# Kernel optimization log

Measured on AMD Instinct MI355X. Metric: run time of the kernel, lower is better.

The kernel has to match this reference:

```python
import jax, jax.numpy as jnp
import numpy as np

# Fixed problem geometry: B equal-sized graphs with contiguous node ids.
B, N, E, F_IN, H, C = 64, 1024, 655360, 128, 128, 10
K1 = int(np.ceil(0.8 * N))    # 820 nodes/graph kept by pool1
K2 = int(np.ceil(0.8 * K1))   # 656 nodes/graph kept by pool2


def setup_inputs() -> dict:
    key = jax.random.key(0)
    ks = jax.random.split(key, 12)
    x = jax.random.normal(ks[0], (B * N, F_IN), jnp.float32)
    # intra-graph random edges, E//B per graph
    e_per = E // B
    local = jax.random.randint(ks[1], (2, E), 0, N)
    off = jnp.repeat(jnp.arange(B, dtype=jnp.int32) * N, e_per)
    edge_index = (local + off[None, :]).astype(jnp.int32)
    batch = jnp.repeat(jnp.arange(B, dtype=jnp.int32), N)

    def lin(k, i, o):
        return jax.random.normal(k, (i, o), jnp.float32) / np.sqrt(i)

    return {
        "x": x, "edge_index": edge_index, "batch": batch,
        "Wl1": lin(ks[2], F_IN, H), "bl1": jnp.zeros((H,), jnp.float32), "Wr1": lin(ks[3], F_IN, H),
        "Wl2": lin(ks[4], H, H),    "bl2": jnp.zeros((H,), jnp.float32), "Wr2": lin(ks[5], H, H),
        "pw1": jax.random.normal(ks[6], (H,), jnp.float32) / np.sqrt(H),
        "pw2": jax.random.normal(ks[7], (H,), jnp.float32) / np.sqrt(H),
        "fW1": lin(ks[8], 2 * H, H), "fb1": jnp.zeros((H,), jnp.float32),
        "fW2": lin(ks[9], H, C),     "fb2": jnp.zeros((C,), jnp.float32),
    }


def _sage(x, src, dst, em, Wl, bl, Wr, n):
    # PyG SAGEConv (aggr='mean'): lin_l(mean_{j->i} x_j) + lin_r(x_i)
    msg = x[src] * em[:, None]                                   # [E, d]
    s = jax.ops.segment_sum(msg, dst, num_segments=n)            # [n, d]
    cnt = jax.ops.segment_sum(em, dst, num_segments=n)           # [n]
    mean = s / jnp.maximum(cnt, 1.0)[:, None]
    return mean @ Wl + bl + x @ Wr


def _topk_pool(x, src, dst, em, n_per, k, w):
    # PyG TopKPooling: score = tanh(x.w/||w||); keep top-k per graph; gate kept x by score.
    score = jnp.tanh(x @ w / jnp.linalg.norm(w))                 # [B*n_per]
    _, idx = jax.lax.top_k(score.reshape(B, n_per), k)           # [B, k]
    idx = jnp.sort(idx, axis=1)
    perm = (idx + (jnp.arange(B) * n_per)[:, None]).reshape(-1)  # global kept ids [B*k]
    nx = x[perm] * score[perm][:, None]
    # relabel edges; drop edges touching removed nodes via mask
    inv = jnp.full((B * n_per,), -1, jnp.int32).at[perm].set(jnp.arange(B * k, dtype=jnp.int32))
    ns, nd = inv[src], inv[dst]
    nm = em * (ns >= 0).astype(x.dtype) * (nd >= 0).astype(x.dtype)
    return nx, jnp.maximum(ns, 0), jnp.maximum(nd, 0), nm


def _readout(h, k):
    g = h.reshape(B, k, H)
    return jnp.concatenate([g.mean(axis=1), g.max(axis=1)], axis=1)  # [B, 2H]


def reference(x, edge_index, batch, Wl1, bl1, Wr1, Wl2, bl2, Wr2,
              pw1, pw2, fW1, fb1, fW2, fb2):
    src, dst = edge_index[0], edge_index[1]
    em = jnp.ones((E,), x.dtype)
    h = jax.nn.relu(_sage(x, src, dst, em, Wl1, bl1, Wr1, B * N))
    h, src, dst, em = _topk_pool(h, src, dst, em, N, K1, pw1)
    x1 = _readout(h, K1)
    h = jax.nn.relu(_sage(h, src, dst, em, Wl2, bl2, Wr2, B * K1))
    h, src, dst, em = _topk_pool(h, src, dst, em, K1, K2, pw2)
    x2 = _readout(h, K2)
    z = jax.nn.relu((x1 + x2) @ fW1 + fb1)
    # dropout is identity in eval mode
    return z @ fW2 + fb2
```

## Files before the change

kernel.cpp:

```cpp
#include <hip/hip_runtime.h>
#include <cstdint>
#include <cstddef>

namespace {

constexpr int kB    = 64;
constexpr int kN    = 1024;
constexpr int kE    = 655360;
constexpr int kEper = kE / kB;
constexpr int kH    = 128;
constexpr int kK1   = 820;
constexpr int kK2   = 656;
constexpr int kM1   = kB * kN;
constexpr int kM2   = kB * kK1;
constexpr int kM3   = kB * kK2;
constexpr int kRChunks = 16;

typedef __attribute__((ext_vector_type(8))) short bf16x8;
typedef __attribute__((ext_vector_type(4))) float f32x4;

__device__ inline ushort f2bf(float f) {
  uint u = __float_as_uint(f);
  return (ushort)((u + 0x7fffu + ((u >> 16) & 1u)) >> 16);
}
__device__ inline float bf2f(ushort s) { return __uint_as_float(((uint)s) << 16); }

__device__ inline void cvt4(const float* f, uint* hh, uint* ll) {
#pragma unroll
  for (int i = 0; i < 2; ++i) {
    uint h;
    asm("v_cvt_pk_bf16_f32 %0, %1, %2" : "=v"(h) : "v"(f[2 * i]), "v"(f[2 * i + 1]));
    const float r0 = __uint_as_float(h << 16);
    const float r1 = __uint_as_float(h & 0xFFFF0000u);
    const float d0 = f[2 * i] - r0;
    const float d1 = f[2 * i + 1] - r1;
    uint l;
    asm("v_cvt_pk_bf16_f32 %0, %1, %2" : "=v"(l) : "v"(d0), "v"(d1));
    hh[i] = h; ll[i] = l;
  }
}

__device__ inline void llds16(const ushort* g, ushort* l) {
  __builtin_amdgcn_global_load_lds(
      (const __attribute__((address_space(1))) void*)g,
      (__attribute__((address_space(3))) void*)l, 16, 0, 0);
}

__device__ inline int block_scan_1024(int v, int* wsum ) {
  const int lane = threadIdx.x & 63;
  const int w    = threadIdx.x >> 6;
#pragma unroll
  for (int off = 1; off < 64; off <<= 1) {
    const int n = __shfl_up(v, off);
    if (lane >= off) v += n;
  }
  if (lane == 63) wsum[w] = v;
  __syncthreads();
  if (w == 0) {
    int s = (lane < 16) ? wsum[lane] : 0;
#pragma unroll
    for (int off = 1; off < 16; off <<= 1) {
      const int n = __shfl_up(s, off);
      if (lane >= off) s += n;
    }
    if (lane < 16) wsum[lane] = s;
  }
  __syncthreads();
  if (w > 0) v += wsum[w - 1];
  return v;
}

__global__ __launch_bounds__(1024)
void build_prep(const int* __restrict__ src, const int* __restrict__ dst,
                int* __restrict__ coff, int* __restrict__ ccur,
                int* __restrict__ ent,
                const float* __restrict__ Wl1, const float* __restrict__ Wr1,
                const float* __restrict__ Wl2, const float* __restrict__ Wr2,
                const float* __restrict__ pw1, const float* __restrict__ pw2,
                ushort* __restrict__ W1h, ushort* __restrict__ W1l,
                ushort* __restrict__ W2h, ushort* __restrict__ W2l,
                float* __restrict__ pwn1, float* __restrict__ pwn2) {
  const int b   = blockIdx.x;
  const int tid = threadIdx.x;
  if (b >= 128) {
    if (tid >= 256) return;
    const float* pw = (tid < 128) ? pw1 : pw2;
    float* o        = (tid < 128) ? pwn1 : pwn2;
    const int j = tid & 127;
    float sum = 0.0f;
    for (int k = 0; k < 128; ++k) { const float v = pw[k]; sum += v * v; }
    o[j] = pw[j] / sqrtf(sum);
    return;
  }
  if (b >= 64) {
    const int ob  = (b - 64) * 4 + (tid >> 8);
    const bool l2 = ob >= 128;
    const int idx = (ob & 127) * 256 + (tid & 255);
    const int n = idx >> 8, k = idx & 255;
    const float* Wl = l2 ? Wl2 : Wl1;
    const float* Wr = l2 ? Wr2 : Wr1;
    const float w = (k < 128) ? Wl[k * kH + n] : Wr[(k - 128) * kH + n];
    const ushort h = f2bf(w);
    (l2 ? W2h : W1h)[n * 256 + k] = h;
    (l2 ? W2l : W1l)[n * 256 + k] = f2bf(w - bf2f(h));
    return;
  }
  __shared__ int cnt[1024];
  __shared__ int wsum[16];
  const int g = b;
  const int ebase = g * kEper;
  cnt[tid] = 0;
  __syncthreads();
  for (int e = tid; e < kEper; e += 1024)
    atomicAdd(&cnt[dst[ebase + e] & (kN - 1)], 1);
  __syncthreads();
  const int dg   = cnt[tid];
  const int incl = block_scan_1024(dg, wsum);
  const int start = ebase + incl - dg;
  coff[g * kN + tid] = start;
  ccur[g * kN + tid] = start + dg;
  __syncthreads();
  cnt[tid] = start;
  __syncthreads();
  for (int e = tid; e < kEper; e += 1024) {
    const int d   = dst[ebase + e] & (kN - 1);
    const int pos = atomicAdd(&cnt[d], 1);
    ent[pos] = src[ebase + e] & (kN - 1);
  }
}

__global__ __launch_bounds__(1024, 8)
void gather1_lds(const float* __restrict__ feat, const int* __restrict__ ent,
                 const int* __restrict__ off, const int* __restrict__ cursor,
                 float* __restrict__ aggout) {
  __shared__ float cache[1024 * 16];
  const int xcd   = blockIdx.x & 7;
  const int local = blockIdx.x >> 3;
  const int graph = xcd * 8 + (local >> 3);
  const int chunk = local & 7;
  const int tid   = threadIdx.x;
  const int gbase = graph << 10;

#pragma unroll
  for (int ps = 0; ps < 4; ++ps) {
    const int row = ps * 256 + (tid >> 2);
    const int q   = (tid & 3) * 4;
    const float4 v = *(const float4*)(feat + (size_t)(gbase + row) * kH + chunk * 16 + q);
    *(float4*)&cache[row * 16 + q] = v;
  }
  __syncthreads();

  const int grp = tid >> 2;
  const int q4  = (tid & 3) * 4;

  for (int it = 0; it < 4; ++it) {
    const int lnode = it * 256 + grp;
    const int node  = gbase + lnode;
    const int o0 = off[node];
    const int o1 = cursor[node];
    const int deg = o1 - o0;
    float4 acc = make_float4(0.f, 0.f, 0.f, 0.f);
    int pf[4];
#pragma unroll
    for (int i = 0; i < 4; ++i) pf[i] = (o0 + i < o1) ? ent[o0 + i] : 0;
    for (int eb = 0; eb < deg; eb += 4) {
      int nx[4];
#pragma unroll
      for (int i = 0; i < 4; ++i) {
        const int idx = o0 + eb + 4 + i;
        nx[i] = (idx < o1) ? ent[idx] : 0;
      }
#pragma unroll
      for (int i = 0; i < 4; ++i) {
        const float m = (eb + i < deg) ? 1.0f : 0.0f;
        const float4 v = *(const float4*)&cache[pf[i] * 16 + q4];
        acc.x = fmaf(v.x, m, acc.x);
        acc.y = fmaf(v.y, m, acc.y);
        acc.z = fmaf(v.z, m, acc.z);
        acc.w = fmaf(v.w, m, acc.w);
      }
#pragma unroll
      for (int i = 0; i < 4; ++i) pf[i] = nx[i];
    }
    const float r = 1.0f / fmaxf((float)deg, 1.0f);
    const f32x4 res = {acc.x * r, acc.y * r, acc.z * r, acc.w * r};
    __builtin_nontemporal_store(res, (f32x4*)(aggout + (size_t)node * kH + chunk * 16 + q4));
  }
}

__global__ __launch_bounds__(1024, 8)
void gather2_lds(const float* __restrict__ feat, const int* __restrict__ ent,
                 const int* __restrict__ off, const int* __restrict__ cursor,
                 const int* __restrict__ perm, const float* __restrict__ gsg,
                 float* __restrict__ aggout) {
  __shared__ float cache[1024 * 16];
  __shared__ float gs[1024];
  const int xcd   = blockIdx.x & 7;
  const int local = blockIdx.x >> 3;
  const int graph = xcd * 8 + (local >> 3);
  const int chunk = local & 7;
  const int tid   = threadIdx.x;
  const int gbase = graph << 10;

#pragma unroll
  for (int ps = 0; ps < 4; ++ps) {
    const int row = ps * 256 + (tid >> 2);
    const int q   = (tid & 3) * 4;
    const float4 v = *(const float4*)(feat + (size_t)(gbase + row) * kH + chunk * 16 + q);
    *(float4*)&cache[row * 16 + q] = v;
  }
  gs[tid] = gsg[gbase + tid];
  __syncthreads();

  const int grp = tid >> 2;
  const int q4  = (tid & 3) * 4;

  for (int it = 0; it < 4; ++it) {
    const int lnode = it * 256 + grp;
    int o0 = 0, o1 = 0;
    if (lnode < kK1) {
      const int orig = perm[graph * kK1 + lnode];
      o0 = off[orig];
      o1 = cursor[orig];
    }
    const int deg = o1 - o0;
    float4 acc = make_float4(0.f, 0.f, 0.f, 0.f);
    int cnt = 0;
    int pf[4];
#pragma unroll
    for (int i = 0; i < 4; ++i) pf[i] = (o0 + i < o1) ? ent[o0 + i] : 0;
    for (int eb = 0; eb < deg; eb += 4) {
      int nx[4];
#pragma unroll
      for (int i = 0; i < 4; ++i) {
        const int idx = o0 + eb + 4 + i;
        nx[i] = (idx < o1) ? ent[idx] : 0;
      }
#pragma unroll
      for (int i = 0; i < 4; ++i) {
        const float raw  = gs[pf[i]];
        const bool  kept = (raw > 0.5f) && (eb + i < deg);
        const float s    = kept ? raw - 2.0f : 0.0f;
        cnt += kept ? 1 : 0;
        const float4 v = *(const float4*)&cache[pf[i] * 16 + q4];
        acc.x = fmaf(v.x, s, acc.x);
        acc.y = fmaf(v.y, s, acc.y);
        acc.z = fmaf(v.z, s, acc.z);
        acc.w = fmaf(v.w, s, acc.w);
      }
#pragma unroll
      for (int i = 0; i < 4; ++i) pf[i] = nx[i];
    }
    const float r = 1.0f / fmaxf((float)cnt, 1.0f);
    const f32x4 res = {acc.x * r, acc.y * r, acc.z * r, acc.w * r};
    if (lnode < kK1)
      __builtin_nontemporal_store(res,
          (f32x4*)(aggout + (size_t)(graph * kK1 + lnode) * kH + chunk * 16 + q4));
  }
}

__global__ __launch_bounds__(256)
void sage_gemm_mfma(const float* __restrict__ meanb, const float* __restrict__ xsrc,
                    const int* __restrict__ perm, const float* __restrict__ gsc,
                    const ushort* __restrict__ WTh, const ushort* __restrict__ WTl,
                    const float* __restrict__ bias, const float* __restrict__ pwn,
                    float* __restrict__ outp, float* __restrict__ scr) {
  __shared__ __align__(16) ushort aH[64][32];
  __shared__ __align__(16) ushort aL[64][32];
  __shared__ __align__(16) ushort wHs[128][32];
  __shared__ __align__(16) ushort wLs[128][32];
  __shared__ float sdot[64][2];
  const int tid  = threadIdx.x;
  const int wid  = tid >> 6;
  const int lane = tid & 63;
  const int quad = lane >> 4;
  const int l16  = lane & 15;
  const int rowbase = blockIdx.x * 64;
  const int wr = (wid >> 1) * 32;
  const int wc = (wid & 1) * 64;

  const int n0a = wid * 32;
  const int n0b = wid * 32 + 16;
  const int wrowa = (n0a + (lane >> 2)) * 256 + (lane & 3) * 8;
  const int wrowb = (n0b + (lane >> 2)) * 256 + (lane & 3) * 8;

  f32x4 acc[2][4];
#pragma unroll
  for (int a = 0; a < 2; ++a)
#pragma unroll
    for (int b = 0; b < 4; ++b) acc[a][b] = (f32x4){0.f, 0.f, 0.f, 0.f};

  for (int s = 0; s < 8; ++s) {
    const bool ismean = s < 4;
    const float* sp = ismean ? meanb : xsrc;
    const int kbase = s * 32;
    const int kloc  = ismean ? kbase : kbase - 128;
#pragma unroll
    for (int i = 0; i < 2; ++i) {
      const int p   = tid + i * 256;
      const int row = p >> 3;
      const int k4  = (p & 7) * 4;
      const int grow = rowbase + row;
      int srow = grow; float scale = 1.0f;
      if (perm) { if (!ismean) { srow = perm[grow]; scale = gsc[grow]; } }
      const float4 v = *(const float4*)(sp + (size_t)srow * kH + kloc + k4);
      float f[4] = {v.x * scale, v.y * scale, v.z * scale, v.w * scale};
      uint hh[2], ll[2];
      cvt4(f, hh, ll);
      *(uint2*)&aH[row][k4] = make_uint2(hh[0], hh[1]);
      *(uint2*)&aL[row][k4] = make_uint2(ll[0], ll[1]);
    }
    llds16(WTh + wrowa + kbase, &wHs[n0a][0]);
    llds16(WTh + wrowb + kbase, &wHs[n0b][0]);
    llds16(WTl + wrowa + kbase, &wLs[n0a][0]);
    llds16(WTl + wrowb + kbase, &wLs[n0b][0]);
    __syncthreads();
    bf16x8 afh[2], afl[2];
#pragma unroll
    for (int rt = 0; rt < 2; ++rt) {
      afh[rt] = *(const bf16x8*)&aH[wr + rt * 16 + l16][quad * 8];
      afl[rt] = *(const bf16x8*)&aL[wr + rt * 16 + l16][quad * 8];
    }
#pragma unroll
    for (int ct = 0; ct < 4; ++ct) {
      const bf16x8 bh = *(const bf16x8*)&wHs[wc + ct * 16 + l16][quad * 8];
      const bf16x8 bl = *(const bf16x8*)&wLs[wc + ct * 16 + l16][quad * 8];
#pragma unroll
      for (int rt = 0; rt < 2; ++rt) {
        acc[rt][ct] = __builtin_amdgcn_mfma_f32_16x16x32_bf16(afh[rt], bh, acc[rt][ct], 0, 0, 0);
        acc[rt][ct] = __builtin_amdgcn_mfma_f32_16x16x32_bf16(afh[rt], bl, acc[rt][ct], 0, 0, 0);
        acc[rt][ct] = __builtin_amdgcn_mfma_f32_16x16x32_bf16(afl[rt], bh, acc[rt][ct], 0, 0, 0);
      }
    }
    __syncthreads();
  }
  float bv[4], pwv[4];
#pragma unroll
  for (int ct = 0; ct < 4; ++ct) {
    const int col = wc + ct * 16 + l16;
    bv[ct]  = bias[col];
    pwv[ct] = pwn[col];
  }
  float dot[2][4];
#pragma unroll
  for (int rt = 0; rt < 2; ++rt)
#pragma unroll
    for (int reg = 0; reg < 4; ++reg) dot[rt][reg] = 0.0f;
#pragma unroll
  for (int ct = 0; ct < 4; ++ct) {
    const int col = wc + ct * 16 + l16;
#pragma unroll
    for (int rt = 0; rt < 2; ++rt) {
#pragma unroll
      for (int reg = 0; reg < 4; ++reg) {
        const int row = rowbase + wr + rt * 16 + quad * 4 + reg;
        const float o = fmaxf(acc[rt][ct][reg] + bv[ct], 0.0f);
        outp[(size_t)row * kH + col] = o;
        dot[rt][reg] += o * pwv[ct];
      }
    }
  }
#pragma unroll
  for (int rt = 0; rt < 2; ++rt) {
#pragma unroll
    for (int reg = 0; reg < 4; ++reg) {
      float d = dot[rt][reg];
      d += __shfl_xor(d, 1);
      d += __shfl_xor(d, 2);
      d += __shfl_xor(d, 4);
      d += __shfl_xor(d, 8);
      if (l16 == 0) sdot[wr + rt * 16 + quad * 4 + reg][wc >> 6] = d;
    }
  }
  __syncthreads();
  if (tid < 64) scr[rowbase + tid] = tanhf(sdot[tid][0] + sdot[tid][1]);
}

__global__ __launch_bounds__(1024)
void rank_compact(const float* __restrict__ scr, int n_per, int K,
                  int* __restrict__ perm, float* __restrict__ gsc,
                  float* __restrict__ gsg) {
  __shared__ int hist[256];
  __shared__ int wsum[16];
  __shared__ uint bT;
  __shared__ int bRem;
  const int g = blockIdx.x, tid = threadIdx.x;
  const float sc = (tid < n_per) ? scr[g * n_per + tid] : -3e30f;
  const uint bits = __float_as_uint(sc);
  const uint key = (bits & 0x80000000u) ? ~bits : (bits | 0x80000000u);

  uint prefix = 0;
  int rem = K;
#pragma unroll
  for (int shift = 24; shift >= 0; shift -= 8) {
    if (tid < 256) hist[tid] = 0;
    __syncthreads();
    const uint mask = (shift == 24) ? 0u : (0xFFFFFFFFu << (shift + 8));
    if ((key & mask) == prefix)
      atomicAdd(&hist[(key >> shift) & 255], 1);
    __syncthreads();
    if (tid < 64) {
      const int h0 = hist[4 * tid + 0], h1 = hist[4 * tid + 1];
      const int h2 = hist[4 * tid + 2], h3 = hist[4 * tid + 3];
      const int loc = h0 + h1 + h2 + h3;
      int suf = loc;
#pragma unroll
      for (int d = 1; d < 64; d <<= 1) {
        const int o = __shfl_down(suf, d);
        if (tid + d < 64) suf += o;
      }
      const int above = suf - loc;
      int hs[5];
      hs[4] = above;
      hs[3] = above + h3;
      hs[2] = hs[3] + h2;
      hs[1] = hs[2] + h1;
      hs[0] = hs[1] + h0;
#pragma unroll
      for (int q = 0; q < 4; ++q) {
        if (hs[q] >= rem && hs[q + 1] < rem) {
          bT   = prefix | ((uint)(4 * tid + q) << shift);
          bRem = rem - hs[q + 1];
        }
      }
    }
    __syncthreads();
    prefix = bT;
    rem    = bRem;
  }
  const int gt = (key > prefix) ? 1 : 0;
  const int eq = (key == prefix) ? 1 : 0;
  const int incl = block_scan_1024((gt << 11) | eq, wsum);
  const int excl = incl - ((gt << 11) | eq);
  const int gt_excl = excl >> 11;
  const int eq_excl = excl & 2047;
  const int keep = (tid < n_per) && (gt || (eq && eq_excl < rem));
  if (keep) {
    const int pos = gt_excl + min(eq_excl, rem);
    perm[g * K + pos] = g * n_per + tid;
    gsc[g * K + pos]  = sc;
  }
  if (gsg) gsg[g * kN + tid] = keep ? sc + 2.0f : 0.0f;
}

__global__ __launch_bounds__(256)
void readout_part(const float* __restrict__ h, const int* __restrict__ perm,
                  const float* __restrict__ gsc, int K,
                  float* __restrict__ psum, float* __restrict__ pmax) {
  const int g     = blockIdx.x >> 4;
  const int chunk = blockIdx.x & (kRChunks - 1);
  const int j     = threadIdx.x & 127;
  const int part  = threadIdx.x >> 7;
  const int rows  = (K + kRChunks - 1) / kRChunks;
  const int r0 = chunk * rows;
  const int r1 = min(r0 + rows, K);
  float sum = 0.0f, mx = -1e30f;
  int r = r0 + part;
  if (r < r1) {
    int   row = perm[g * K + r];
    float sc  = gsc[g * K + r];
    while (r < r1) {
      const int rn = r + 2;
      int   row_n = 0;
      float sc_n  = 0.0f;
      if (rn < r1) { row_n = perm[g * K + rn]; sc_n = gsc[g * K + rn]; }
      const float v = h[(size_t)row * kH + j] * sc;
      sum += v;
      mx = fmaxf(mx, v);
      row = row_n; sc = sc_n; r = rn;
    }
  }
  __shared__ float ss[2][128], sm[2][128];
  ss[part][j] = sum;
  sm[part][j] = mx;
  __syncthreads();
  if (part == 0) {
    sum += ss[1][j];
    mx = fmaxf(mx, sm[1][j]);
    psum[(size_t)blockIdx.x * 128 + j] = sum;
    pmax[(size_t)blockIdx.x * 128 + j] = mx;
  }
}

__global__ __launch_bounds__(128)
void final_mlp(const float* __restrict__ ps1, const float* __restrict__ pm1,
               const float* __restrict__ ps2, const float* __restrict__ pm2,
               const float* __restrict__ fW1, const float* __restrict__ fb1,
               const float* __restrict__ fW2, const float* __restrict__ fb2,
               float* __restrict__ out) {
  __shared__ float xx[256];
  __shared__ float z[128];
  const int g = blockIdx.x, tid = threadIdx.x;
  float s1 = 0.f, m1 = -1e30f, s2 = 0.f, m2 = -1e30f;
#pragma unroll
  for (int c = 0; c < kRChunks; ++c) {
    s1 += ps1[(size_t)(g * kRChunks + c) * 128 + tid];
    m1 = fmaxf(m1, pm1[(size_t)(g * kRChunks + c) * 128 + tid]);
    s2 += ps2[(size_t)(g * kRChunks + c) * 128 + tid];
    m2 = fmaxf(m2, pm2[(size_t)(g * kRChunks + c) * 128 + tid]);
  }
  xx[tid]       = s1 / (float)kK1 + s2 / (float)kK2;
  xx[tid + 128] = m1 + m2;
  __syncthreads();
  float a = fb1[tid];
  for (int k = 0; k < 256; ++k) a += xx[k] * fW1[k * 128 + tid];
  z[tid] = fmaxf(a, 0.0f);
  __syncthreads();
  if (tid < 10) {
    float o = fb2[tid];
    for (int k = 0; k < 128; ++k) o += z[k] * fW2[k * 10 + tid];
    out[g * 10 + tid] = o;
  }
}

}

extern "C" void kernel_launch(void* const* d_in, const int* in_sizes, int n_in,
                              void* d_out, int out_size, void* d_ws, size_t ws_size,
                              hipStream_t stream) {
  const float* x   = (const float*)d_in[0];
  const int*   ei  = (const int*)d_in[1];
  const float* Wl1 = (const float*)d_in[3];
  const float* bl1 = (const float*)d_in[4];
  const float* Wr1 = (const float*)d_in[5];
  const float* Wl2 = (const float*)d_in[6];
  const float* bl2 = (const float*)d_in[7];
  const float* Wr2 = (const float*)d_in[8];
  const float* pw1 = (const float*)d_in[9];
  const float* pw2 = (const float*)d_in[10];
  const float* fW1 = (const float*)d_in[11];
  const float* fb1 = (const float*)d_in[12];
  const float* fW2 = (const float*)d_in[13];
  const float* fb2 = (const float*)d_in[14];
  const int* src = ei;
  const int* dst = ei + kE;
  (void)in_sizes; (void)n_in; (void)out_size; (void)ws_size;

  char* wsb = (char*)d_ws;
  size_t off_b = 0;
  auto alloc = [&](size_t bytes) {
    void* p = wsb + off_b;
    off_b += (bytes + 255) & ~(size_t)255;
    return p;
  };
  float* bufA = (float*)alloc((size_t)kM1 * kH * 4);
  float* bufB = (float*)alloc((size_t)kM1 * kH * 4);
  float* bufC = (float*)alloc((size_t)kM2 * kH * 4);
  int*   coff = (int*)alloc((size_t)kM1 * 4);
  int*   ccur = (int*)alloc((size_t)kM1 * 4);
  int*   ent  = (int*)alloc((size_t)kE * 4);
  float* scr  = (float*)alloc((size_t)kM1 * 4);
  float* gsg  = (float*)alloc((size_t)kM1 * 4);
  int*   perm1= (int*)alloc((size_t)kM2 * 4);
  float* gsc1 = (float*)alloc((size_t)kM2 * 4);
  int*   perm2= (int*)alloc((size_t)kM3 * 4);
  float* gsc2 = (float*)alloc((size_t)kM3 * 4);
  float* psum1= (float*)alloc((size_t)kB * kRChunks * 128 * 4);
  float* pmax1= (float*)alloc((size_t)kB * kRChunks * 128 * 4);
  float* psum2= (float*)alloc((size_t)kB * kRChunks * 128 * 4);
  float* pmax2= (float*)alloc((size_t)kB * kRChunks * 128 * 4);
  ushort* wt1h = (ushort*)alloc((size_t)128 * 256 * 2);
  ushort* wt1l = (ushort*)alloc((size_t)128 * 256 * 2);
  ushort* wt2h = (ushort*)alloc((size_t)128 * 256 * 2);
  ushort* wt2l = (ushort*)alloc((size_t)128 * 256 * 2);
  float* pwn1 = (float*)alloc(128 * 4);
  float* pwn2 = (float*)alloc(128 * 4);

  build_prep<<<129, 1024, 0, stream>>>(src, dst, coff, ccur, ent,
                                       Wl1, Wr1, Wl2, Wr2, pw1, pw2,
                                       wt1h, wt1l, wt2h, wt2l, pwn1, pwn2);

  gather1_lds<<<kB * 8, 1024, 0, stream>>>(x, ent, coff, ccur, bufA);
  sage_gemm_mfma<<<kM1 / 64, 256, 0, stream>>>(bufA, x, nullptr, nullptr,
                                               wt1h, wt1l, bl1, pwn1, bufB, scr);
  rank_compact<<<kB, 1024, 0, stream>>>(scr, kN, kK1, perm1, gsc1, gsg);
  readout_part<<<kB * kRChunks, 256, 0, stream>>>(bufB, perm1, gsc1, kK1, psum1, pmax1);

  gather2_lds<<<kB * 8, 1024, 0, stream>>>(bufB, ent, coff, ccur, perm1, gsg, bufA);
  sage_gemm_mfma<<<kM2 / 64, 256, 0, stream>>>(bufA, bufB, perm1, gsc1,
                                               wt2h, wt2l, bl2, pwn2, bufC, scr);
  rank_compact<<<kB, 1024, 0, stream>>>(scr, kK1, kK2, perm2, gsc2, nullptr);
  readout_part<<<kB * kRChunks, 256, 0, stream>>>(bufC, perm2, gsc2, kK2, psum2, pmax2);

  final_mlp<<<kB, 128, 0, stream>>>(psum1, pmax1, psum2, pmax2,
                                    fW1, fb1, fW2, fb2, (float*)d_out);
}
```

Baseline: 256.8 us.

## Fuse pool1 readout into gather2 and use direct global-to-LDS loads

Removes the separate readout_part kernel for the first pooling stage. gather2 already holds the whole graph's feature chunk in LDS, so it now also computes the per-graph sum and max of the gated kept nodes and writes them out. Both gather kernels now fill their LDS cache with global_load_lds instead of going through registers. The sage GEMM also hoists the perm and scale lookups out of its k-loop. This drops one launch and one pass over bufB, at the cost of some extra reduction work and a barrier at the end of gather2.

```diff
diff --git a/kernel.cpp b/kernel.cpp
--- a/kernel.cpp
+++ b/kernel.cpp
@@ -40,7 +40,7 @@
   }
 }
 
-__device__ inline void llds16(const ushort* g, ushort* l) {
+__device__ inline void llds16(const void* g, void* l) {
   __builtin_amdgcn_global_load_lds(
       (const __attribute__((address_space(1))) void*)g,
       (__attribute__((address_space(3))) void*)l, 16, 0, 0);
@@ -139,14 +139,15 @@
   const int graph = xcd * 8 + (local >> 3);
   const int chunk = local & 7;
   const int tid   = threadIdx.x;
+  const int wid   = tid >> 6;
   const int gbase = graph << 10;
 
 #pragma unroll
   for (int ps = 0; ps < 4; ++ps) {
     const int row = ps * 256 + (tid >> 2);
     const int q   = (tid & 3) * 4;
-    const float4 v = *(const float4*)(feat + (size_t)(gbase + row) * kH + chunk * 16 + q);
-    *(float4*)&cache[row * 16 + q] = v;
+    llds16(feat + (size_t)(gbase + row) * kH + chunk * 16 + q,
+           cache + ps * 4096 + wid * 256);
   }
   __syncthreads();
 
@@ -192,22 +193,25 @@
 void gather2_lds(const float* __restrict__ feat, const int* __restrict__ ent,
                  const int* __restrict__ off, const int* __restrict__ cursor,
                  const int* __restrict__ perm, const float* __restrict__ gsg,
-                 float* __restrict__ aggout) {
+                 float* __restrict__ aggout,
+                 float* __restrict__ psumg, float* __restrict__ pmaxg) {
   __shared__ float cache[1024 * 16];
   __shared__ float gs[1024];
+  __shared__ float rps[16][16], rpm[16][16];
   const int xcd   = blockIdx.x & 7;
   const int local = blockIdx.x >> 3;
   const int graph = xcd * 8 + (local >> 3);
   const int chunk = local & 7;
   const int tid   = threadIdx.x;
+  const int wid   = tid >> 6;
   const int gbase = graph << 10;
 
 #pragma unroll
   for (int ps = 0; ps < 4; ++ps) {
     const int row = ps * 256 + (tid >> 2);
     const int q   = (tid & 3) * 4;
-    const float4 v = *(const float4*)(feat + (size_t)(gbase + row) * kH + chunk * 16 + q);
-    *(float4*)&cache[row * 16 + q] = v;
+    llds16(feat + (size_t)(gbase + row) * kH + chunk * 16 + q,
+           cache + ps * 4096 + wid * 256);
   }
   gs[tid] = gsg[gbase + tid];
   __syncthreads();
@@ -256,6 +260,32 @@
     if (lnode < kK1)
       __builtin_nontemporal_store(res,
           (f32x4*)(aggout + (size_t)(graph * kK1 + lnode) * kH + chunk * 16 + q4));
+  }
+
+  __syncthreads();
+  const int rcol = tid & 15;
+  const int rseg = tid >> 4;
+  float rs = 0.0f, rm = -1e30f;
+#pragma unroll
+  for (int i = 0; i < 16; ++i) {
+    const int row = rseg * 16 + i;
+    const float raw = gs[row];
+    if (raw > 0.5f) {
+      const float v = cache[row * 16 + rcol] * (raw - 2.0f);
+      rs += v;
+      rm = fmaxf(rm, v);
+    }
+  }
+  rs += __shfl_xor(rs, 16); rs += __shfl_xor(rs, 32);
+  rm = fmaxf(rm, __shfl_xor(rm, 16)); rm = fmaxf(rm, __shfl_xor(rm, 32));
+  if ((tid & 48) == 0) { rps[wid][rcol] = rs; rpm[wid][rcol] = rm; }
+  __syncthreads();
+  if (tid < 16) {
+    float ts = 0.0f, tm = -1e30f;
+#pragma unroll
+    for (int w = 0; w < 16; ++w) { ts += rps[w][tid]; tm = fmaxf(tm, rpm[w][tid]); }
+    psumg[graph * kH + chunk * 16 + tid] = ts;
+    pmaxg[graph * kH + chunk * 16 + tid] = tm;
   }
 }
 
@@ -284,6 +314,14 @@
   const int wrowa = (n0a + (lane >> 2)) * 256 + (lane & 3) * 8;
   const int wrowb = (n0b + (lane >> 2)) * 256 + (lane & 3) * 8;
 
+  int srow1[2]; float scl1[2];
+#pragma unroll
+  for (int i = 0; i < 2; ++i) {
+    const int grow = rowbase + ((tid + i * 256) >> 3);
+    srow1[i] = grow; scl1[i] = 1.0f;
+    if (perm) { srow1[i] = perm[grow]; scl1[i] = gsc[grow]; }
+  }
+
   f32x4 acc[2][4];
 #pragma unroll
   for (int a = 0; a < 2; ++a)
@@ -300,9 +338,8 @@
       const int p   = tid + i * 256;
       const int row = p >> 3;
       const int k4  = (p & 7) * 4;
-      const int grow = rowbase + row;
-      int srow = grow; float scale = 1.0f;
-      if (perm) { if (!ismean) { srow = perm[grow]; scale = gsc[grow]; } }
+      const int srow   = ismean ? (rowbase + row) : srow1[i];
+      const float scale = ismean ? 1.0f : scl1[i];
       const float4 v = *(const float4*)(sp + (size_t)srow * kH + kloc + k4);
       float f[4] = {v.x * scale, v.y * scale, v.z * scale, v.w * scale};
       uint hh[2], ll[2];
@@ -491,11 +528,11 @@
   __shared__ float xx[256];
   __shared__ float z[128];
   const int g = blockIdx.x, tid = threadIdx.x;
-  float s1 = 0.f, m1 = -1e30f, s2 = 0.f, m2 = -1e30f;
+  const float s1 = ps1[(size_t)g * 128 + tid];
+  const float m1 = pm1[(size_t)g * 128 + tid];
+  float s2 = 0.f, m2 = -1e30f;
 #pragma unroll
   for (int c = 0; c < kRChunks; ++c) {
-    s1 += ps1[(size_t)(g * kRChunks + c) * 128 + tid];
-    m1 = fmaxf(m1, pm1[(size_t)(g * kRChunks + c) * 128 + tid]);
     s2 += ps2[(size_t)(g * kRChunks + c) * 128 + tid];
     m2 = fmaxf(m2, pm2[(size_t)(g * kRChunks + c) * 128 + tid]);
   }
@@ -555,8 +592,8 @@
   float* gsc1 = (float*)alloc((size_t)kM2 * 4);
   int*   perm2= (int*)alloc((size_t)kM3 * 4);
   float* gsc2 = (float*)alloc((size_t)kM3 * 4);
-  float* psum1= (float*)alloc((size_t)kB * kRChunks * 128 * 4);
-  float* pmax1= (float*)alloc((size_t)kB * kRChunks * 128 * 4);
+  float* psum1= (float*)alloc((size_t)kB * 128 * 4);
+  float* pmax1= (float*)alloc((size_t)kB * 128 * 4);
   float* psum2= (float*)alloc((size_t)kB * kRChunks * 128 * 4);
   float* pmax2= (float*)alloc((size_t)kB * kRChunks * 128 * 4);
   ushort* wt1h = (ushort*)alloc((size_t)128 * 256 * 2);
@@ -574,9 +611,9 @@
   sage_gemm_mfma<<<kM1 / 64, 256, 0, stream>>>(bufA, x, nullptr, nullptr,
                                                wt1h, wt1l, bl1, pwn1, bufB, scr);
   rank_compact<<<kB, 1024, 0, stream>>>(scr, kN, kK1, perm1, gsc1, gsg);
-  readout_part<<<kB * kRChunks, 256, 0, stream>>>(bufB, perm1, gsc1, kK1, psum1, pmax1);
-
-  gather2_lds<<<kB * 8, 1024, 0, stream>>>(bufB, ent, coff, ccur, perm1, gsg, bufA);
+
+  gather2_lds<<<kB * 8, 1024, 0, stream>>>(bufB, ent, coff, ccur, perm1, gsg,
+                                           bufA, psum1, pmax1);
   sage_gemm_mfma<<<kM2 / 64, 256, 0, stream>>>(bufA, bufB, perm1, gsc1,
                                                wt2h, wt2l, bl2, pwn2, bufC, scr);
   rank_compact<<<kB, 1024, 0, stream>>>(scr, kK1, kK2, perm2, gsc2, nullptr);
```

Measured after the change: 250.1 us. 1.03x faster.
